# Performance work log

Measured on AMD Instinct MI355X. Metric: run time of the kernel, lower is better.

The kernel has to match this reference:

```python
import jax, jax.numpy as jnp
import numpy as np

D_MODEL = 1024
NUM_HEADS = 16
HEAD_DIM = D_MODEL // NUM_HEADS


def setup_inputs() -> dict:
    key = jax.random.key(0)
    ks = jax.random.split(key, 11)
    B, S = 2, 2048
    s = 1.0 / np.sqrt(D_MODEL)
    inp = {
        "query": jax.random.normal(ks[0], (B, S, D_MODEL), jnp.float32),
        "key": jax.random.normal(ks[1], (B, S, D_MODEL), jnp.float32),
        "value": jax.random.normal(ks[2], (B, S, D_MODEL), jnp.float32),
        "Wq": jax.random.normal(ks[3], (D_MODEL, D_MODEL), jnp.float32) * s,
        "bq": jnp.zeros((D_MODEL,), jnp.float32),
        "Wk": jax.random.normal(ks[4], (D_MODEL, D_MODEL), jnp.float32) * s,
        "bk": jnp.zeros((D_MODEL,), jnp.float32),
        "Wv": jax.random.normal(ks[5], (D_MODEL, D_MODEL), jnp.float32) * s,
        "bv": jnp.zeros((D_MODEL,), jnp.float32),
        "Wo": jax.random.normal(ks[6], (D_MODEL, D_MODEL), jnp.float32) * s,
        "bo": jnp.zeros((D_MODEL,), jnp.float32),
    }
    return inp


def _split_heads(x):
    B, S, _ = x.shape
    return x.reshape(B, S, NUM_HEADS, HEAD_DIM).transpose(0, 2, 1, 3)  # [B,H,S,d]


def reference(query, key, value, Wq, bq, Wk, bk, Wv, bv, Wo, bo):
    Q = _split_heads(query @ Wq.T + bq)
    K = _split_heads(key @ Wk.T + bk)
    V = _split_heads(value @ Wv.T + bv)
    scale = 1.0 / jnp.sqrt(jnp.asarray(HEAD_DIM, jnp.float32))
    scores = jnp.einsum("bhqd,bhkd->bhqk", Q, K) * scale  # [B,H,S,S]
    weights = jax.nn.softmax(scores, axis=-1)
    attn = jnp.einsum("bhqk,bhkd->bhqd", weights, V)
    B, H, S, d = attn.shape
    attn = attn.transpose(0, 2, 1, 3).reshape(B, S, H * d)
    return attn @ Wo.T + bo
```

## Files before the change

### kernel.cpp

```cpp
#include <hip/hip_runtime.h>
#include <hip/hip_bf16.h>


typedef unsigned short u16;
typedef __attribute__((ext_vector_type(8))) short short8;
typedef __attribute__((ext_vector_type(4))) float floatx4;

__device__ __forceinline__ float bf2f(u16 x) {
  return __uint_as_float(((unsigned)x) << 16);
}
__device__ __forceinline__ u16 f2bf(float f) {
  unsigned x = __float_as_uint(f);
  return (u16)((x + 0x7fffu + ((x >> 16) & 1u)) >> 16);
}
__device__ __forceinline__ ushort2 pk_bf16(float a, float b) {
  __hip_bfloat162 h2 = __float22bfloat162_rn(make_float2(a, b));
  ushort2 u;
  __builtin_memcpy(&u, &h2, 4);
  return u;
}
#if __has_builtin(__builtin_amdgcn_exp2f)
#define EXP2(x) __builtin_amdgcn_exp2f(x)
#else
#define EXP2(x) exp2f(x)
#endif
__device__ __forceinline__ void gll16(const u16* g, u16* lds) {
  __builtin_amdgcn_global_load_lds((const __attribute__((address_space(1))) void*)g,
                                   (__attribute__((address_space(3))) void*)lds,
                                   16, 0, 0);
}

__global__ __launch_bounds__(256) void cvt_kernel(
    const float* __restrict__ q, const float* __restrict__ k, const float* __restrict__ v,
    const float* __restrict__ wq, const float* __restrict__ wk,
    const float* __restrict__ wv, const float* __restrict__ wo,
    const float* __restrict__ bq, const float* __restrict__ bk,
    const float* __restrict__ bv, const float* __restrict__ bo,
    u16* __restrict__ ws) {
  const int i4 = (blockIdx.x * 256 + threadIdx.x) * 4;
  const float* src;
  u16* dst;
  int local;
  if (i4 < 4194304)        { src = q;  dst = ws;            local = i4; }
  else if (i4 < 8388608)   { src = k;  dst = ws + 4194304;  local = i4 - 4194304; }
  else if (i4 < 12582912)  { src = v;  dst = ws + 8388608;  local = i4 - 8388608; }
  else if (i4 < 13631488)  { src = wq; dst = ws + 12582912; local = i4 - 12582912; }
  else if (i4 < 14680064)  { src = wk; dst = ws + 13631488; local = i4 - 13631488; }
  else if (i4 < 15728640)  { src = wv; dst = ws + 14680064; local = i4 - 14680064; }
  else if (i4 < 16777216)  { src = wo; dst = ws + 15728640; local = i4 - 15728640; }
  else if (i4 < 16778240)  { src = bq; dst = ws + 16777216; local = i4 - 16777216; }
  else if (i4 < 16779264)  { src = bk; dst = ws + 16779264; local = i4 - 16778240; }
  else if (i4 < 16780288)  { src = bv; dst = ws + 16781312; local = i4 - 16779264; }
  else                     { src = bo; dst = ws + 16783360; local = i4 - 16780288; }
  const float4 f = *(const float4*)(src + local);
  ushort4 o;
  o.x = f2bf(f.x); o.y = f2bf(f.y); o.z = f2bf(f.z); o.w = f2bf(f.w);
  *(ushort4*)(dst + local) = o;
}

template <int MTILE>
__device__ __forceinline__ void gemm_tile(
    const u16* __restrict__ X, const u16* __restrict__ W,
    const u16* __restrict__ bias, u16* __restrict__ out16, float* __restrict__ out32,
    int row0, int col0, int mode, float oscale, u16* As, u16* Bs) {
  constexpr int NI = MTILE / 32;
  constexpr int ABUF = MTILE * 32;
  const int tid = threadIdx.x;
  const int w = tid >> 6, l = tid & 63;
  const int lan = l & 15, quad = l >> 4;
  const int wm = w & 1, wn = w >> 1;

  floatx4 acc[NI][4];
#pragma unroll
  for (int i = 0; i < NI; ++i)
#pragma unroll
    for (int j = 0; j < 4; ++j) acc[i][j] = (floatx4)0.0f;

  const int r0 = tid >> 2, kq0 = tid & 3;
  const int r1 = (tid + 256) >> 2;
  const int woff = w * 512;
  const u16* Xa0 = X + (size_t)(row0 + r0) * 1024 + kq0 * 8;
  const u16* Xa1 = X + (size_t)(row0 + (MTILE == 128 ? r1 : r0)) * 1024 + kq0 * 8;
  const u16* Wb0 = W + (size_t)(col0 + r0) * 1024 + kq0 * 8;
  const u16* Wb1 = W + (size_t)(col0 + r1) * 1024 + kq0 * 8;

#define STAGE(buf, kt)                                           \
  do {                                                           \
    gll16(Xa0 + (kt) * 32, As + (buf) * ABUF + woff);            \
    if (MTILE == 128)                                            \
      gll16(Xa1 + (kt) * 32, As + (buf) * ABUF + 2048 + woff);   \
    gll16(Wb0 + (kt) * 32, Bs + (buf) * 4096 + woff);            \
    gll16(Wb1 + (kt) * 32, Bs + (buf) * 4096 + 2048 + woff);     \
  } while (0)

  STAGE(0, 0);
  int cur = 0;
  for (int kt = 0; kt < 32; ++kt) {
    if (kt < 31) {
      const int nb = cur == 2 ? 0 : cur + 1;
      STAGE(nb, kt + 1);
      if (MTILE == 128)
        __asm__ volatile("s_waitcnt vmcnt(4)" ::: "memory");
      else
        __asm__ volatile("s_waitcnt vmcnt(3)" ::: "memory");
    } else {
      __asm__ volatile("s_waitcnt vmcnt(0)" ::: "memory");
    }
    __builtin_amdgcn_s_barrier();

    const u16* Ab = As + cur * ABUF;
    const u16* Bb = Bs + cur * 4096;
    short8 af[NI], bfr[4];
#pragma unroll
    for (int i = 0; i < NI; ++i)
      af[i] = *(const short8*)(Ab + (wm * (MTILE / 2) + i * 16 + lan) * 32 + quad * 8);
#pragma unroll
    for (int j = 0; j < 4; ++j)
      bfr[j] = *(const short8*)(Bb + (wn * 64 + j * 16 + lan) * 32 + quad * 8);
#pragma unroll
    for (int i = 0; i < NI; ++i)
#pragma unroll
      for (int j = 0; j < 4; ++j)
        acc[i][j] = __builtin_amdgcn_mfma_f32_16x16x32_bf16(af[i], bfr[j], acc[i][j], 0, 0, 0);
    cur = cur == 2 ? 0 : cur + 1;
  }
#undef STAGE

#pragma unroll
  for (int i = 0; i < NI; ++i) {
    const int mb = row0 + wm * (MTILE / 2) + i * 16 + quad * 4;
#pragma unroll
    for (int j = 0; j < 4; ++j) {
      const int n = col0 + wn * 64 + j * 16 + lan;
      const float bv = bf2f(bias[n]);
      if (mode == 0) {
#pragma unroll
        for (int r = 0; r < 4; ++r)
          out16[(size_t)(mb + r) * 1024 + n] = f2bf((acc[i][j][r] + bv) * oscale);
      } else if (mode == 1) {
        const int b = mb >> 11;
        const int h = n >> 6, dd = n & 63;
        u16* base = out16 + (size_t)((b * 16 + h) * 64 + dd) * 2048;
        const int s0 = mb & 2047;
        const int k0 = s0 & 63;
        const int sp0 = (s0 & ~63) | (((k0 >> 5) & 1) << 5) | (((k0 >> 2) & 3) << 3) |
                        (((k0 >> 4) & 1) << 2);
        ushort4 ov;
        ov.x = f2bf(acc[i][j][0] + bv);
        ov.y = f2bf(acc[i][j][1] + bv);
        ov.z = f2bf(acc[i][j][2] + bv);
        ov.w = f2bf(acc[i][j][3] + bv);
        *(ushort4*)(base + sp0) = ov;
      } else {
#pragma unroll
        for (int r = 0; r < 4; ++r)
          out32[(size_t)(mb + r) * 1024 + n] = acc[i][j][r] + bv;
      }
    }
  }
}

__global__ __launch_bounds__(256) void qkv_kernel(
    const u16* __restrict__ xq, const u16* __restrict__ xk, const u16* __restrict__ xv,
    const u16* __restrict__ Wq, const u16* __restrict__ Wk, const u16* __restrict__ Wv,
    const u16* __restrict__ bq, const u16* __restrict__ bk, const u16* __restrict__ bv,
    u16* __restrict__ Qo, u16* __restrict__ Ko, u16* __restrict__ Vto) {
  __shared__ __align__(16) u16 As[3 * 4096];
  __shared__ __align__(16) u16 Bs[3 * 4096];
  const int bx = blockIdx.x;
  const int xcd = bx & 7;
  const int j = bx >> 3;
  const int c = j & 7;
  const int gidx = j >> 3;
  const int g = gidx * 8 + xcd;
  const int which = g >> 5;
  const int tile_m = g & 31;
  const int col0 = c * 128;
  const u16* X = which == 0 ? xq : (which == 1 ? xk : xv);
  const u16* W = which == 0 ? Wq : (which == 1 ? Wk : Wv);
  const u16* bias = which == 0 ? bq : (which == 1 ? bk : bv);
  u16* out = which == 0 ? Qo : (which == 1 ? Ko : Vto);
  const float C = 0.125f * 1.4426950408889634f;
  gemm_tile<128>(X, W, bias, out, nullptr, tile_m * 128, col0, which == 2 ? 1 : 0,
                 which == 0 ? C : 1.0f, As, Bs);
}

__global__ __launch_bounds__(256) void proj_kernel(
    const u16* __restrict__ X, const u16* __restrict__ W,
    const u16* __restrict__ bias, float* __restrict__ out) {
  __shared__ __align__(16) u16 As[3 * 2048];
  __shared__ __align__(16) u16 Bs[3 * 4096];
  const int bx = blockIdx.x;
  const int xcd = bx & 7;
  const int j = bx >> 3;
  const int c = j & 7;
  const int gidx = j >> 3;
  const int tm = xcd * 8 + gidx;
  gemm_tile<64>(X, W, bias, nullptr, out, tm * 64, c * 128, 2, 1.0f, As, Bs);
}

#define FIXMAX 16.0f
#define KPAD 72
__global__ __launch_bounds__(256, 2) void attn_kernel(
    const u16* __restrict__ Q, const u16* __restrict__ K,
    const u16* __restrict__ Vt, u16* __restrict__ O) {
  __shared__ __align__(16) u16 KV[4][64 * KPAD];
  const int tid = threadIdx.x;
  const int w = tid >> 6, l = tid & 63;
  const int lan = l & 15, quad = l >> 4;
  const int g = w >> 1;
  const int h2 = w & 1;
  const int id = blockIdx.x + (blockIdx.y << 4);
  const int xcd = id & 7;
  const int jj = id >> 3;
  const int bh = xcd * 4 + (jj >> 4);
  const int q0 = (jj & 15) * 128;
  const int b = bh >> 4, h = bh & 15;
  const u16* Qg = Q + (size_t)(b * 2048 + q0) * 1024 + h * 64;
  const u16* Kg = K + (size_t)(b * 2048) * 1024 + h * 64;
  const u16* Vg = Vt + (size_t)((b * 16 + h) * 64) * 2048;

  short8 qf[4][2];
#pragma unroll
  for (int mi = 0; mi < 4; ++mi)
#pragma unroll
    for (int kk = 0; kk < 2; ++kk)
      qf[mi][kk] = *(const short8*)(Qg + (size_t)(g * 64 + mi * 16 + lan) * 1024 +
                                    kk * 32 + quad * 8);

  float lrun[4] = {0.f, 0.f, 0.f, 0.f};
  floatx4 oacc[4][4];
#pragma unroll
  for (int mi = 0; mi < 4; ++mi)
#pragma unroll
    for (int nd = 0; nd < 4; ++nd) oacc[mi][nd] = (floatx4)0.0f;

  const int rowA = tid >> 3, colq = (tid & 7) * 8;
  const int rowB = rowA + 32;

  short8 k0 = *(const short8*)(Kg + (size_t)rowA * 1024 + colq);
  short8 k1 = *(const short8*)(Kg + (size_t)rowB * 1024 + colq);
  short8 v0 = *(const short8*)(Vg + (size_t)rowA * 2048 + colq);
  short8 v1 = *(const short8*)(Vg + (size_t)rowB * 2048 + colq);
  *(short8*)(KV[0] + rowA * KPAD + colq) = k0;
  *(short8*)(KV[0] + rowB * KPAD + colq) = k1;
  *(short8*)(KV[2] + rowA * KPAD + colq) = v0;
  *(short8*)(KV[2] + rowB * KPAD + colq) = v1;
  __syncthreads();

  for (int kt = 0; kt < 32; ++kt) {
    const int cur = kt & 1;
    if (kt < 31) {
      const int kn = kt + 1;
      k0 = *(const short8*)(Kg + (size_t)(kn * 64 + rowA) * 1024 + colq);
      k1 = *(const short8*)(Kg + (size_t)(kn * 64 + rowB) * 1024 + colq);
      v0 = *(const short8*)(Vg + (size_t)rowA * 2048 + kn * 64 + colq);
      v1 = *(const short8*)(Vg + (size_t)rowB * 2048 + kn * 64 + colq);
    }
    const u16* Kc = KV[cur];
    const u16* Vc = KV[2 + cur];

    floatx4 sacc[4][2];
#pragma unroll
    for (int mi = 0; mi < 4; ++mi)
#pragma unroll
      for (int nj2 = 0; nj2 < 2; ++nj2) sacc[mi][nj2] = (floatx4)(-FIXMAX);
#pragma unroll
    for (int kk = 0; kk < 2; ++kk) {
      short8 kf[2];
#pragma unroll
      for (int nj2 = 0; nj2 < 2; ++nj2)
        kf[nj2] = *(const short8*)(Kc + ((2 * h2 + nj2) * 16 + lan) * KPAD +
                                   kk * 32 + quad * 8);
      __builtin_amdgcn_s_setprio(1);
#pragma unroll
      for (int mi = 0; mi < 4; ++mi)
#pragma unroll
        for (int nj2 = 0; nj2 < 2; ++nj2)
          sacc[mi][nj2] = __builtin_amdgcn_mfma_f32_16x16x32_bf16(
              kf[nj2], qf[mi][kk], sacc[mi][nj2], 0, 0, 0);
      __builtin_amdgcn_s_setprio(0);
    }

    short8 vf[4];
#pragma unroll
    for (int nd = 0; nd < 4; ++nd)
      vf[nd] = *(const short8*)(Vc + (nd * 16 + lan) * KPAD + h2 * 32 + quad * 8);

    short8 pb[4];
#pragma unroll
    for (int mi = 0; mi < 4; ++mi) {
      float p[2][4];
#pragma unroll
      for (int nj2 = 0; nj2 < 2; ++nj2)
#pragma unroll
        for (int r = 0; r < 4; ++r) p[nj2][r] = EXP2(sacc[mi][nj2][r]);
      float s0 = 0.f, s1 = 0.f;
#pragma unroll
      for (int r = 0; r < 4; ++r) {
        s0 += p[0][r];
        s1 += p[1][r];
      }
      lrun[mi] += s0 + s1;
      const ushort2 w0 = pk_bf16(p[0][0], p[0][1]);
      const ushort2 w1 = pk_bf16(p[0][2], p[0][3]);
      const ushort2 w2 = pk_bf16(p[1][0], p[1][1]);
      const ushort2 w3 = pk_bf16(p[1][2], p[1][3]);
      union { short8 s8; ushort us[8]; } u;
      u.us[0] = w0.x; u.us[1] = w0.y; u.us[2] = w1.x; u.us[3] = w1.y;
      u.us[4] = w2.x; u.us[5] = w2.y; u.us[6] = w3.x; u.us[7] = w3.y;
      pb[mi] = u.s8;
    }

    __builtin_amdgcn_s_setprio(1);
#pragma unroll
    for (int mi = 0; mi < 4; ++mi)
#pragma unroll
      for (int nd = 0; nd < 4; ++nd)
        oacc[mi][nd] = __builtin_amdgcn_mfma_f32_16x16x32_bf16(
            vf[nd], pb[mi], oacc[mi][nd], 0, 0, 0);
    __builtin_amdgcn_s_setprio(0);

    if (kt < 31) {
      const int nxt = cur ^ 1;
      *(short8*)(KV[nxt] + rowA * KPAD + colq) = k0;
      *(short8*)(KV[nxt] + rowB * KPAD + colq) = k1;
      *(short8*)(KV[2 + nxt] + rowA * KPAD + colq) = v0;
      *(short8*)(KV[2 + nxt] + rowB * KPAD + colq) = v1;
      __syncthreads();
    }
  }

#pragma unroll
  for (int mi = 0; mi < 4; ++mi) {
    lrun[mi] += __shfl_xor(lrun[mi], 16);
    lrun[mi] += __shfl_xor(lrun[mi], 32);
  }
  __syncthreads();
  float4* obuf = (float4*)&KV[0][0];
  float* lbuf = (float*)&KV[0][0] + 8192;
  if (h2 == 1) {
#pragma unroll
    for (int mi = 0; mi < 4; ++mi) {
#pragma unroll
      for (int nd = 0; nd < 4; ++nd) {
        const int fi = mi * 4 + nd;
        float4 t;
        t.x = oacc[mi][nd][0]; t.y = oacc[mi][nd][1];
        t.z = oacc[mi][nd][2]; t.w = oacc[mi][nd][3];
        obuf[(g * 64 + l) * 16 + ((fi + l) & 15)] = t;
      }
      lbuf[(g * 64 + l) * 4 + mi] = lrun[mi];
    }
  }
  __syncthreads();
  if (h2 == 0) {
#pragma unroll
    for (int mi = 0; mi < 4; ++mi) {
      const float lt = lrun[mi] + lbuf[(g * 64 + l) * 4 + mi];
      const float inv = 1.0f / lt;
      const int qg = b * 2048 + q0 + g * 64 + mi * 16 + lan;
#pragma unroll
      for (int nd = 0; nd < 4; ++nd) {
        const int fi = mi * 4 + nd;
        const float4 t = obuf[(g * 64 + l) * 16 + ((fi + l) & 15)];
        ushort4 ov;
        ov.x = f2bf((oacc[mi][nd][0] + t.x) * inv);
        ov.y = f2bf((oacc[mi][nd][1] + t.y) * inv);
        ov.z = f2bf((oacc[mi][nd][2] + t.z) * inv);
        ov.w = f2bf((oacc[mi][nd][3] + t.w) * inv);
        *(ushort4*)(O + (size_t)qg * 1024 + h * 64 + nd * 16 + quad * 4) = ov;
      }
    }
  }
}

extern "C" void kernel_launch(void* const* d_in, const int* in_sizes, int n_in,
                              void* d_out, int out_size, void* d_ws, size_t ws_size,
                              hipStream_t stream) {
  const float* query = (const float*)d_in[0];
  const float* key_ = (const float*)d_in[1];
  const float* value = (const float*)d_in[2];
  const float* Wq = (const float*)d_in[3];
  const float* bq = (const float*)d_in[4];
  const float* Wk = (const float*)d_in[5];
  const float* bk = (const float*)d_in[6];
  const float* Wv = (const float*)d_in[7];
  const float* bv = (const float*)d_in[8];
  const float* Wo = (const float*)d_in[9];
  const float* bo = (const float*)d_in[10];
  float* out = (float*)d_out;

  u16* ws = (u16*)d_ws;
  u16* Xq = ws;
  u16* Xk = ws + 4194304;
  u16* Xv = ws + 8388608;
  u16* cWq = ws + 12582912;
  u16* cWk = ws + 13631488;
  u16* cWv = ws + 14680064;
  u16* cWo = ws + 15728640;
  u16* cbq = ws + 16777216;
  u16* cbk = ws + 16779264;
  u16* cbv = ws + 16781312;
  u16* cbo = ws + 16783360;
  u16* Qw = ws + 17301504;
  u16* Kw = ws + 21495808;
  u16* Vtw = ws + 25690112;
  u16* Ow = ws + 29884416;

  cvt_kernel<<<16388, 256, 0, stream>>>(query, key_, value, Wq, Wk, Wv, Wo,
                                        bq, bk, bv, bo, ws);
  qkv_kernel<<<768, 256, 0, stream>>>(Xq, Xk, Xv, cWq, cWk, cWv, cbq, cbk, cbv,
                                      Qw, Kw, Vtw);
  attn_kernel<<<dim3(16, 32), 256, 0, stream>>>(Qw, Kw, Vtw, Ow);
  proj_kernel<<<512, 256, 0, stream>>>(Ow, cWo, cbo, out);
}
```

Before: 217.7 us.

## Fuse fp32-to-bf16 activation conversion into QKV GEMM A-tile staging

Removes the separate conversion pass over the query/key/value activations. The QKV GEMM now loads fp32 activation rows straight into registers, converts them to bf16, and writes them into shared memory after the MFMA step, overlapping that work with the async weight loads. This avoids writing and re-reading 12M bf16 values through global memory. In exchange it adds register pressure, VALU conversion work, and explicit LDS writes inside the GEMM main loop, plus reworked waitcnt logic.

```diff
diff --git a/kernel.cpp b/kernel.cpp
--- a/kernel.cpp
+++ b/kernel.cpp
@@ -18,6 +18,14 @@
   ushort2 u;
   __builtin_memcpy(&u, &h2, 4);
   return u;
+}
+__device__ __forceinline__ short8 cvt8(float4 a, float4 b) {
+  const ushort2 p0 = pk_bf16(a.x, a.y), p1 = pk_bf16(a.z, a.w);
+  const ushort2 p2 = pk_bf16(b.x, b.y), p3 = pk_bf16(b.z, b.w);
+  union { short8 s8; ushort us[8]; } u;
+  u.us[0] = p0.x; u.us[1] = p0.y; u.us[2] = p1.x; u.us[3] = p1.y;
+  u.us[4] = p2.x; u.us[5] = p2.y; u.us[6] = p3.x; u.us[7] = p3.y;
+  return u.s8;
 }
 #if __has_builtin(__builtin_amdgcn_exp2f)
 #define EXP2(x) __builtin_amdgcn_exp2f(x)
@@ -31,7 +39,6 @@
 }
 
 __global__ __launch_bounds__(256) void cvt_kernel(
-    const float* __restrict__ q, const float* __restrict__ k, const float* __restrict__ v,
     const float* __restrict__ wq, const float* __restrict__ wk,
     const float* __restrict__ wv, const float* __restrict__ wo,
     const float* __restrict__ bq, const float* __restrict__ bk,
@@ -41,27 +48,25 @@
   const float* src;
   u16* dst;
   int local;
-  if (i4 < 4194304)        { src = q;  dst = ws;            local = i4; }
-  else if (i4 < 8388608)   { src = k;  dst = ws + 4194304;  local = i4 - 4194304; }
-  else if (i4 < 12582912)  { src = v;  dst = ws + 8388608;  local = i4 - 8388608; }
-  else if (i4 < 13631488)  { src = wq; dst = ws + 12582912; local = i4 - 12582912; }
-  else if (i4 < 14680064)  { src = wk; dst = ws + 13631488; local = i4 - 13631488; }
-  else if (i4 < 15728640)  { src = wv; dst = ws + 14680064; local = i4 - 14680064; }
-  else if (i4 < 16777216)  { src = wo; dst = ws + 15728640; local = i4 - 15728640; }
-  else if (i4 < 16778240)  { src = bq; dst = ws + 16777216; local = i4 - 16777216; }
-  else if (i4 < 16779264)  { src = bk; dst = ws + 16779264; local = i4 - 16778240; }
-  else if (i4 < 16780288)  { src = bv; dst = ws + 16781312; local = i4 - 16779264; }
-  else                     { src = bo; dst = ws + 16783360; local = i4 - 16780288; }
+  if (i4 < 1048576)       { src = wq; dst = ws + 12582912; local = i4; }
+  else if (i4 < 2097152)  { src = wk; dst = ws + 13631488; local = i4 - 1048576; }
+  else if (i4 < 3145728)  { src = wv; dst = ws + 14680064; local = i4 - 2097152; }
+  else if (i4 < 4194304)  { src = wo; dst = ws + 15728640; local = i4 - 3145728; }
+  else if (i4 < 4195328)  { src = bq; dst = ws + 16777216; local = i4 - 4194304; }
+  else if (i4 < 4196352)  { src = bk; dst = ws + 16779264; local = i4 - 4195328; }
+  else if (i4 < 4197376)  { src = bv; dst = ws + 16781312; local = i4 - 4196352; }
+  else                    { src = bo; dst = ws + 16783360; local = i4 - 4197376; }
   const float4 f = *(const float4*)(src + local);
   ushort4 o;
   o.x = f2bf(f.x); o.y = f2bf(f.y); o.z = f2bf(f.z); o.w = f2bf(f.w);
   *(ushort4*)(dst + local) = o;
 }
 
-template <int MTILE>
+template <int MTILE, bool XF32>
 __device__ __forceinline__ void gemm_tile(
-    const u16* __restrict__ X, const u16* __restrict__ W,
-    const u16* __restrict__ bias, u16* __restrict__ out16, float* __restrict__ out32,
+    const u16* __restrict__ X16, const float* __restrict__ X32,
+    const u16* __restrict__ W, const u16* __restrict__ bias,
+    u16* __restrict__ out16, float* __restrict__ out32,
     int row0, int col0, int mode, float oscale, u16* As, u16* Bs) {
   constexpr int NI = MTILE / 32;
   constexpr int ABUF = MTILE * 32;
@@ -79,32 +84,56 @@
   const int r0 = tid >> 2, kq0 = tid & 3;
   const int r1 = (tid + 256) >> 2;
   const int woff = w * 512;
-  const u16* Xa0 = X + (size_t)(row0 + r0) * 1024 + kq0 * 8;
-  const u16* Xa1 = X + (size_t)(row0 + (MTILE == 128 ? r1 : r0)) * 1024 + kq0 * 8;
+  const u16* Xa0 = XF32 ? nullptr : X16 + (size_t)(row0 + r0) * 1024 + kq0 * 8;
+  const float* Xf0 = XF32 ? X32 + (size_t)(row0 + r0) * 1024 + kq0 * 8 : nullptr;
+  const float* Xf1 = XF32 ? X32 + (size_t)(row0 + r1) * 1024 + kq0 * 8 : nullptr;
   const u16* Wb0 = W + (size_t)(col0 + r0) * 1024 + kq0 * 8;
   const u16* Wb1 = W + (size_t)(col0 + r1) * 1024 + kq0 * 8;
 
-#define STAGE(buf, kt)                                           \
+#define STAGEW(buf, kt)                                          \
   do {                                                           \
-    gll16(Xa0 + (kt) * 32, As + (buf) * ABUF + woff);            \
-    if (MTILE == 128)                                            \
-      gll16(Xa1 + (kt) * 32, As + (buf) * ABUF + 2048 + woff);   \
     gll16(Wb0 + (kt) * 32, Bs + (buf) * 4096 + woff);            \
     gll16(Wb1 + (kt) * 32, Bs + (buf) * 4096 + 2048 + woff);     \
   } while (0)
-
-  STAGE(0, 0);
+#define STAGEXG(buf, kt)                                         \
+  do {                                                           \
+    gll16(Xa0 + (kt) * 32, As + (buf) * ABUF + woff);            \
+  } while (0)
+
+  float4 xl0a, xl0b, xl1a, xl1b;
+  if (XF32) {
+    xl0a = *(const float4*)(Xf0 + 0);
+    xl0b = *(const float4*)(Xf0 + 4);
+    xl1a = *(const float4*)(Xf1 + 0);
+    xl1b = *(const float4*)(Xf1 + 4);
+    STAGEW(0, 0);
+    *(short8*)(As + tid * 8) = cvt8(xl0a, xl0b);
+    *(short8*)(As + 2048 + tid * 8) = cvt8(xl1a, xl1b);
+  } else {
+    STAGEXG(0, 0);
+    STAGEW(0, 0);
+  }
   int cur = 0;
   for (int kt = 0; kt < 32; ++kt) {
+    const int nb = cur == 2 ? 0 : cur + 1;
     if (kt < 31) {
-      const int nb = cur == 2 ? 0 : cur + 1;
-      STAGE(nb, kt + 1);
-      if (MTILE == 128)
-        __asm__ volatile("s_waitcnt vmcnt(4)" ::: "memory");
+      if (XF32) {
+        xl0a = *(const float4*)(Xf0 + (kt + 1) * 32);
+        xl0b = *(const float4*)(Xf0 + (kt + 1) * 32 + 4);
+        xl1a = *(const float4*)(Xf1 + (kt + 1) * 32);
+        xl1b = *(const float4*)(Xf1 + (kt + 1) * 32 + 4);
+        STAGEW(nb, kt + 1);
+        __asm__ volatile("s_waitcnt vmcnt(6) lgkmcnt(0)" ::: "memory");
+      } else {
+        STAGEXG(nb, kt + 1);
+        STAGEW(nb, kt + 1);
+        __asm__ volatile("s_waitcnt vmcnt(3)" ::: "memory");
+      }
+    } else {
+      if (XF32)
+        __asm__ volatile("s_waitcnt vmcnt(0) lgkmcnt(0)" ::: "memory");
       else
-        __asm__ volatile("s_waitcnt vmcnt(3)" ::: "memory");
-    } else {
-      __asm__ volatile("s_waitcnt vmcnt(0)" ::: "memory");
+        __asm__ volatile("s_waitcnt vmcnt(0)" ::: "memory");
     }
     __builtin_amdgcn_s_barrier();
 
@@ -122,9 +151,15 @@
 #pragma unroll
       for (int j = 0; j < 4; ++j)
         acc[i][j] = __builtin_amdgcn_mfma_f32_16x16x32_bf16(af[i], bfr[j], acc[i][j], 0, 0, 0);
-    cur = cur == 2 ? 0 : cur + 1;
-  }
-#undef STAGE
+
+    if (XF32 && kt < 31) {
+      *(short8*)(As + nb * ABUF + tid * 8) = cvt8(xl0a, xl0b);
+      *(short8*)(As + nb * ABUF + 2048 + tid * 8) = cvt8(xl1a, xl1b);
+    }
+    cur = nb;
+  }
+#undef STAGEW
+#undef STAGEXG
 
 #pragma unroll
   for (int i = 0; i < NI; ++i) {
@@ -161,7 +196,8 @@
 }
 
 __global__ __launch_bounds__(256) void qkv_kernel(
-    const u16* __restrict__ xq, const u16* __restrict__ xk, const u16* __restrict__ xv,
+    const float* __restrict__ xq, const float* __restrict__ xk,
+    const float* __restrict__ xv,
     const u16* __restrict__ Wq, const u16* __restrict__ Wk, const u16* __restrict__ Wv,
     const u16* __restrict__ bq, const u16* __restrict__ bk, const u16* __restrict__ bv,
     u16* __restrict__ Qo, u16* __restrict__ Ko, u16* __restrict__ Vto) {
@@ -176,13 +212,13 @@
   const int which = g >> 5;
   const int tile_m = g & 31;
   const int col0 = c * 128;
-  const u16* X = which == 0 ? xq : (which == 1 ? xk : xv);
+  const float* X = which == 0 ? xq : (which == 1 ? xk : xv);
   const u16* W = which == 0 ? Wq : (which == 1 ? Wk : Wv);
   const u16* bias = which == 0 ? bq : (which == 1 ? bk : bv);
   u16* out = which == 0 ? Qo : (which == 1 ? Ko : Vto);
   const float C = 0.125f * 1.4426950408889634f;
-  gemm_tile<128>(X, W, bias, out, nullptr, tile_m * 128, col0, which == 2 ? 1 : 0,
-                 which == 0 ? C : 1.0f, As, Bs);
+  gemm_tile<128, true>(nullptr, X, W, bias, out, nullptr, tile_m * 128, col0,
+                       which == 2 ? 1 : 0, which == 0 ? C : 1.0f, As, Bs);
 }
 
 __global__ __launch_bounds__(256) void proj_kernel(
@@ -196,7 +232,8 @@
   const int c = j & 7;
   const int gidx = j >> 3;
   const int tm = xcd * 8 + gidx;
-  gemm_tile<64>(X, W, bias, nullptr, out, tm * 64, c * 128, 2, 1.0f, As, Bs);
+  gemm_tile<64, false>(X, nullptr, W, bias, nullptr, out, tm * 64, c * 128, 2,
+                       1.0f, As, Bs);
 }
 
 #define FIXMAX 16.0f
@@ -392,9 +429,6 @@
   float* out = (float*)d_out;
 
   u16* ws = (u16*)d_ws;
-  u16* Xq = ws;
-  u16* Xk = ws + 4194304;
-  u16* Xv = ws + 8388608;
   u16* cWq = ws + 12582912;
   u16* cWk = ws + 13631488;
   u16* cWv = ws + 14680064;
@@ -408,10 +442,9 @@
   u16* Vtw = ws + 25690112;
   u16* Ow = ws + 29884416;
 
-  cvt_kernel<<<16388, 256, 0, stream>>>(query, key_, value, Wq, Wk, Wv, Wo,
-                                        bq, bk, bv, bo, ws);
-  qkv_kernel<<<768, 256, 0, stream>>>(Xq, Xk, Xv, cWq, cWk, cWv, cbq, cbk, cbv,
-                                      Qw, Kw, Vtw);
+  cvt_kernel<<<4100, 256, 0, stream>>>(Wq, Wk, Wv, Wo, bq, bk, bv, bo, ws);
+  qkv_kernel<<<768, 256, 0, stream>>>(query, key_, value, cWq, cWk, cWv,
+                                      cbq, cbk, cbv, Qw, Kw, Vtw);
   attn_kernel<<<dim3(16, 32), 256, 0, stream>>>(Qw, Kw, Vtw, Ow);
   proj_kernel<<<512, 256, 0, stream>>>(Ow, cWo, cbo, out);
 }
```

Result: slower. 225.2 us (+3.4%).
